# Performance work log

Measured on AMD Instinct MI355X. Metric: run time of the kernel, lower is better.

## Reference

```python
import jax, jax.numpy as jnp
import numpy as np

H = 64
NG = 100000   # gene nodes
ND = 30000    # disease nodes
NE = 1500000  # gda edges (gene -> disease)
NL = 500000   # supervision (label) edges


def setup_inputs() -> dict:
    key = jax.random.key(0)
    ks = jax.random.split(key, 20)
    s = 0.1
    inp = {
        "gene_emb":    jax.random.normal(ks[0], (NG, H), jnp.float32) * s,
        "disease_emb": jax.random.normal(ks[1], (ND, H), jnp.float32) * s,
    }
    wnames = ["w1_gd_l", "w1_gd_r", "w1_dg_l", "w1_dg_r",
              "w2_gd_l", "w2_gd_r", "w2_dg_l", "w2_dg_r"]
    for i, n in enumerate(wnames):
        inp[n] = jax.random.normal(ks[2 + i], (H, H), jnp.float32) * s
    for i, n in enumerate(["b1_gd", "b1_dg", "b2_gd", "b2_dg"]):
        inp[n] = jax.random.normal(ks[10 + i], (H,), jnp.float32) * 0.01
    inp["edge_src"]  = jax.random.randint(ks[14], (NE,), 0, NG)
    inp["edge_dst"]  = jax.random.randint(ks[15], (NE,), 0, ND)
    inp["label_src"] = jax.random.randint(ks[16], (NL,), 0, NG)
    inp["label_dst"] = jax.random.randint(ks[17], (NL,), 0, ND)
    return inp


def _sage(x_src, x_dst, src, dst, n_dst, wl, wr, b):
    # SAGEConv (mean aggr): lin_l(mean_{j in N(i)} x_j) + lin_r(x_i) + b
    msum = jax.ops.segment_sum(x_src[src], dst, num_segments=n_dst)
    cnt = jax.ops.segment_sum(jnp.ones((src.shape[0], 1), x_src.dtype), dst,
                              num_segments=n_dst)
    mean = msum / jnp.maximum(cnt, 1.0)
    return mean @ wl + x_dst @ wr + b


def reference(gene_emb, disease_emb,
              w1_gd_l, w1_gd_r, b1_gd, w1_dg_l, w1_dg_r, b1_dg,
              w2_gd_l, w2_gd_r, b2_gd, w2_dg_l, w2_dg_r, b2_dg,
              edge_src, edge_dst, label_src, label_dst):
    # layer 1 (hetero: gene->disease via gda, disease->gene via rev_gda)
    h_d = jax.nn.relu(_sage(gene_emb, disease_emb, edge_src, edge_dst, ND,
                            w1_gd_l, w1_gd_r, b1_gd))
    h_g = jax.nn.relu(_sage(disease_emb, gene_emb, edge_dst, edge_src, NG,
                            w1_dg_l, w1_dg_r, b1_dg))
    # layer 2 (no activation)
    h_d2 = _sage(h_g, h_d, edge_src, edge_dst, ND, w2_gd_l, w2_gd_r, b2_gd)
    h_g2 = _sage(h_d, h_g, edge_dst, edge_src, NG, w2_dg_l, w2_dg_r, b2_dg)
    # classifier: dot product over label edges
    return jnp.sum(h_g2[label_src] * h_d2[label_dst], axis=-1)
```

## Files before the change

kernel.cpp:

```cpp
#include <hip/hip_runtime.h>
#include <hip/hip_bf16.h>

#define H 64
#define SCAN_CHUNK 512
#define NB1 512

typedef unsigned short u16;
typedef unsigned int u32;
typedef unsigned char u8;
typedef __attribute__((ext_vector_type(8))) __bf16 bf16x8;
typedef __attribute__((ext_vector_type(4))) float f32x4;
typedef __attribute__((ext_vector_type(2))) float f32x2;

__device__ __forceinline__ float bflo(u32 u) {
    return __builtin_bit_cast(float, u << 16);
}
__device__ __forceinline__ float bfhi(u32 u) {
    return __builtin_bit_cast(float, u & 0xffff0000u);
}
__device__ __forceinline__ u16 bf16rne(float f) {
    u32 u = __builtin_bit_cast(u32, f);
    return (u16)((u + 0x7FFFu + ((u >> 16) & 1u)) >> 16);
}
__device__ __forceinline__ u8 fp8enc(float f) {
    return (u8)(__builtin_amdgcn_cvt_pk_fp8_f32(f, 0.0f, 0, false) & 0xFF);
}

__global__ __launch_bounds__(256) void fused_count_convert_kernel(
    const int* __restrict__ es, const int* __restrict__ ed,
    int* __restrict__ histD, int* __restrict__ histG,
    int ne, int shiftD, int shiftG,
    const float* __restrict__ a, u16* __restrict__ oa, u32* __restrict__ oa8,
    long long na4,
    const float* __restrict__ b, u16* __restrict__ ob, u32* __restrict__ ob8,
    long long nb4)
{
    if (blockIdx.x < NB1) {
        __shared__ int lhd[256], lhg[256];
        const int tid = threadIdx.x;
        lhd[tid] = 0; lhg[tid] = 0;
        __syncthreads();
        const int chunk = (ne + NB1 - 1) / NB1;
        const int e0 = blockIdx.x * chunk;
        const int e1 = min(e0 + chunk, ne);
        for (int e = e0 + tid; e < e1; e += 256) {
            atomicAdd(&lhd[ed[e] >> shiftD], 1);
            atomicAdd(&lhg[es[e] >> shiftG], 1);
        }
        __syncthreads();
        histD[tid * NB1 + blockIdx.x] = lhd[tid];
        histG[tid * NB1 + blockIdx.x] = lhg[tid];
        return;
    }
    long long i = (long long)(blockIdx.x - NB1) * 256 + threadIdx.x;
    const float* src; u16* dst; u32* dst8; long long q;
    if (i < na4) { src = a; dst = oa; dst8 = oa8; q = i; }
    else if (i < na4 + nb4) { src = b; dst = ob; dst8 = ob8; q = i - na4; }
    else return;
    float4 v = *(const float4*)&src[q * 4];
    ushort4 o;
    o.x = bf16rne(v.x); o.y = bf16rne(v.y);
    o.z = bf16rne(v.z); o.w = bf16rne(v.w);
    *(ushort4*)&dst[q * 4] = o;
    int r = 0;
    r = __builtin_amdgcn_cvt_pk_fp8_f32(v.x * 16.0f, v.y * 16.0f, r, false);
    r = __builtin_amdgcn_cvt_pk_fp8_f32(v.z * 16.0f, v.w * 16.0f, r, true);
    dst8[q] = (u32)r;
}

__global__ __launch_bounds__(256) void scan_reduce_kernel(
    const int* __restrict__ a1, int n1, const int* __restrict__ a2, int n2,
    int B1, int* __restrict__ partial,
    u32* __restrict__ pad0, u32* __restrict__ pad1,
    u32* __restrict__ pad2, u32* __restrict__ pad3)
{
    if (blockIdx.x == 0) {
        int tz = threadIdx.x;
        if (tz < 16) pad0[tz] = 0;
        else if (tz < 32) pad1[tz - 16] = 0;
        else if (tz < 48) pad2[tz - 32] = 0;
        else if (tz < 64) pad3[tz - 48] = 0;
    }
    const int b = blockIdx.x;
    const int* a; int n, base;
    if (b < B1) { a = a1; n = n1; base = b * SCAN_CHUNK; }
    else        { a = a2; n = n2; base = (b - B1) * SCAN_CHUNK; }
    int t = threadIdx.x;
    int i0 = base + 2 * t, i1 = i0 + 1;
    int v = ((i0 < n) ? a[i0] : 0) + ((i1 < n) ? a[i1] : 0);
    #pragma unroll
    for (int off = 32; off > 0; off >>= 1) v += __shfl_down(v, off, 64);
    __shared__ int ws[4];
    if ((t & 63) == 0) ws[t >> 6] = v;
    __syncthreads();
    if (t == 0) partial[b] = ws[0] + ws[1] + ws[2] + ws[3];
}

__global__ __launch_bounds__(256) void scan_apply_kernel(
    const int* __restrict__ a1, int* __restrict__ out1, int n1,
    const int* __restrict__ a2, int* __restrict__ out2, int n2,
    int B1, int nbtot, const int* __restrict__ partial)
{
    __shared__ int sExcl[1024];
    __shared__ int ws[4];
    const int tid = threadIdx.x;
    const int lane = tid & 63, wid = tid >> 6;

    int j0 = 4 * tid;
    int p0 = (j0 + 0 < nbtot) ? partial[j0 + 0] : 0;
    int p1 = (j0 + 1 < nbtot) ? partial[j0 + 1] : 0;
    int p2 = (j0 + 2 < nbtot) ? partial[j0 + 2] : 0;
    int p3 = (j0 + 3 < nbtot) ? partial[j0 + 3] : 0;
    int psum = p0 + p1 + p2 + p3;
    int P = psum;
    #pragma unroll
    for (int off = 1; off < 64; off <<= 1) {
        int u = __shfl_up(P, off, 64);
        if (lane >= off) P += u;
    }
    if (lane == 63) ws[wid] = P;
    __syncthreads();
    int wbase = 0;
    #pragma unroll
    for (int w = 0; w < 4; ++w) wbase += (w < wid) ? ws[w] : 0;
    int e = wbase + (P - psum);
    sExcl[j0 + 0] = e;
    sExcl[j0 + 1] = e + p0;
    sExcl[j0 + 2] = e + p0 + p1;
    sExcl[j0 + 3] = e + p0 + p1 + p2;
    __syncthreads();

    const int b = blockIdx.x;
    int tot1 = sExcl[B1 - 1] + partial[B1 - 1];
    int myOff = sExcl[b] - ((b >= B1) ? tot1 : 0);
    if (b == 0 && tid == 0) {
        int tot2 = sExcl[nbtot - 1] + partial[nbtot - 1] - tot1;
        out1[n1] = tot1;
        out2[n2] = tot2;
    }
    __syncthreads();

    const int* a; int* out; int n, base;
    if (b < B1) { a = a1; out = out1; n = n1; base = b * SCAN_CHUNK; }
    else        { a = a2; out = out2; n = n2; base = (b - B1) * SCAN_CHUNK; }
    int i0 = base + 2 * tid, i1 = i0 + 1;
    int x0 = (i0 < n) ? a[i0] : 0;
    int x1 = (i1 < n) ? a[i1] : 0;
    int p = x0 + x1;
    int Q = p;
    #pragma unroll
    for (int off = 1; off < 64; off <<= 1) {
        int u = __shfl_up(Q, off, 64);
        if (lane >= off) Q += u;
    }
    if (lane == 63) ws[wid] = Q;
    __syncthreads();
    int waveBase = 0;
    #pragma unroll
    for (int w = 0; w < 4; ++w) waveBase += (w < wid) ? ws[w] : 0;
    int off0 = myOff + waveBase + (Q - p);
    if (i0 < n) out[i0] = off0;
    if (i1 < n) out[i1] = off0 + x0;
}

__global__ __launch_bounds__(256) void part_scatter_kernel(
    const int* __restrict__ es, const int* __restrict__ ed,
    const int* __restrict__ baseD, const int* __restrict__ baseG,
    u32* __restrict__ pairD, u32* __restrict__ pairG,
    int ne, int shiftD, int shiftG)
{
    __shared__ int curD[256], curG[256];
    const int tid = threadIdx.x;
    curD[tid] = baseD[tid * NB1 + blockIdx.x];
    curG[tid] = baseG[tid * NB1 + blockIdx.x];
    __syncthreads();
    const int maskD = (1 << shiftD) - 1;
    const int maskG = (1 << shiftG) - 1;
    const int chunk = (ne + NB1 - 1) / NB1;
    const int e0 = blockIdx.x * chunk;
    const int e1 = min(e0 + chunk, ne);
    for (int e = e0 + tid; e < e1; e += 256) {
        int s = es[e], d = ed[e];
        int pD = atomicAdd(&curD[d >> shiftD], 1);
        pairD[pD] = ((u32)(d & maskD) << 17) | (u32)s;
        int pG = atomicAdd(&curG[s >> shiftG], 1);
        pairG[pG] = ((u32)(s & maskG) << 17) | (u32)d;
    }
}

__global__ __launch_bounds__(256) void csr_build_kernel(
    const u32* __restrict__ pairD, const int* __restrict__ baseD,
    int* __restrict__ rowD, int* __restrict__ idxD, int nd, int shiftD, int nbktD,
    const u32* __restrict__ pairG, const int* __restrict__ baseG,
    int* __restrict__ rowG, int* __restrict__ idxG, int ng, int shiftG, int nbktG)
{
    __shared__ int lcnt[512], lcur[512];
    __shared__ int ws[4];
    const int j = blockIdx.x & 255;
    const int isG = blockIdx.x >> 8;
    const u32* pair; const int* base; int* row; int* idx; int n, shift, nbkt;
    if (isG) { pair = pairG; base = baseG; row = rowG; idx = idxG; n = ng; shift = shiftG; nbkt = nbktG; }
    else     { pair = pairD; base = baseD; row = rowD; idx = idxD; n = nd; shift = shiftD; nbkt = nbktD; }
    if (j >= nbkt) return;

    const int tid = threadIdx.x;
    const int nLo = j << shift;
    const int nHi = min(nLo + (1 << shift), n);
    const int range = nHi - nLo;
    const int segBase = base[j * NB1];
    const int segEnd  = base[(j + 1) * NB1];

    lcnt[tid] = 0; lcnt[tid + 256] = 0;
    __syncthreads();
    for (int t = segBase + tid; t < segEnd; t += 256)
        atomicAdd(&lcnt[pair[t] >> 17], 1);
    __syncthreads();

    int i0 = 2 * tid, i1 = i0 + 1;
    int c0 = (i0 < range) ? lcnt[i0] : 0;
    int c1 = (i1 < range) ? lcnt[i1] : 0;
    int p = c0 + c1;
    int P = p;
    const int lane = tid & 63, wid = tid >> 6;
    #pragma unroll
    for (int off = 1; off < 64; off <<= 1) {
        int u = __shfl_up(P, off, 64);
        if (lane >= off) P += u;
    }
    if (lane == 63) ws[wid] = P;
    __syncthreads();
    int waveBase = 0;
    #pragma unroll
    for (int w = 0; w < 4; ++w) waveBase += (w < wid) ? ws[w] : 0;
    int o0 = segBase + waveBase + (P - p);
    int o1 = o0 + c0;
    if (i0 < range) { row[nLo + i0] = o0; lcur[i0] = o0; }
    if (i1 < range) { row[nLo + i1] = o1; lcur[i1] = o1; }
    if (nHi == n && tid == 0) row[n] = segEnd;
    __syncthreads();

    for (int t = segBase + tid; t < segEnd; t += 256) {
        u32 pr = pair[t];
        int pos = atomicAdd(&lcur[pr >> 17], 1);
        idx[pos] = (int)(pr & 0x1FFFFu);
    }
}

__global__ __launch_bounds__(256) void gather_mean_kernel(
    const u8* __restrict__ srcD, const u8* __restrict__ srcG,
    const int* __restrict__ rowD, const int* __restrict__ idxD,
    const int* __restrict__ rowG, const int* __restrict__ idxG,
    u16* __restrict__ outD, u16* __restrict__ outG, int nd, int ng)
{
    int hw = blockIdx.x * 8 + (threadIdx.x >> 5);
    int l5 = threadIdx.x & 31;
    if (hw >= nd + ng) return;
    const bool isD = hw < nd;
    const int sub = l5 >> 3;
    const int c8 = l5 & 7;
    const u8* src; const int* row; const int* idx; u16* out; int node, npad;
    if (isD) { src = srcD; row = rowD; idx = idxD; out = outD; node = hw;      npad = ng; }
    else     { src = srcG; row = rowG; idx = idxG; out = outG; node = hw - nd; npad = nd; }
    int beg = row[node], end = row[node + 1];
    const u8* srcc = src + c8 * 8;

    f32x2 aA[4], aB[4];
    #pragma unroll
    for (int j = 0; j < 4; ++j) {
        aA[j] = (f32x2){0.f, 0.f}; aB[j] = (f32x2){0.f, 0.f};
    }

    for (int i = beg; i < end; i += 32) {
        int p = i + sub;
        const int* ip = idx + p;
        int t0 = ip[0],  t1 = ip[4],  t2 = ip[8],  t3 = ip[12];
        int t4 = ip[16], t5 = ip[20], t6 = ip[24], t7 = ip[28];
        int s0 = (p      < end) ? t0 : npad;
        int s1 = (p + 4  < end) ? t1 : npad;
        int s2 = (p + 8  < end) ? t2 : npad;
        int s3 = (p + 12 < end) ? t3 : npad;
        int s4 = (p + 16 < end) ? t4 : npad;
        int s5 = (p + 20 < end) ? t5 : npad;
        int s6 = (p + 24 < end) ? t6 : npad;
        int s7 = (p + 28 < end) ? t7 : npad;
        uint2 v0 = *(const uint2*)(srcc + (size_t)s0 * 64);
        uint2 v1 = *(const uint2*)(srcc + (size_t)s1 * 64);
        uint2 v2 = *(const uint2*)(srcc + (size_t)s2 * 64);
        uint2 v3 = *(const uint2*)(srcc + (size_t)s3 * 64);
        uint2 v4 = *(const uint2*)(srcc + (size_t)s4 * 64);
        uint2 v5 = *(const uint2*)(srcc + (size_t)s5 * 64);
        uint2 v6 = *(const uint2*)(srcc + (size_t)s6 * 64);
        uint2 v7 = *(const uint2*)(srcc + (size_t)s7 * 64);
        aA[0] += __builtin_amdgcn_cvt_pk_f32_fp8((int)v0.x, false);
        aA[1] += __builtin_amdgcn_cvt_pk_f32_fp8((int)v0.x, true);
        aA[2] += __builtin_amdgcn_cvt_pk_f32_fp8((int)v0.y, false);
        aA[3] += __builtin_amdgcn_cvt_pk_f32_fp8((int)v0.y, true);
        aA[0] += __builtin_amdgcn_cvt_pk_f32_fp8((int)v1.x, false);
        aA[1] += __builtin_amdgcn_cvt_pk_f32_fp8((int)v1.x, true);
        aA[2] += __builtin_amdgcn_cvt_pk_f32_fp8((int)v1.y, false);
        aA[3] += __builtin_amdgcn_cvt_pk_f32_fp8((int)v1.y, true);
        aA[0] += __builtin_amdgcn_cvt_pk_f32_fp8((int)v2.x, false);
        aA[1] += __builtin_amdgcn_cvt_pk_f32_fp8((int)v2.x, true);
        aA[2] += __builtin_amdgcn_cvt_pk_f32_fp8((int)v2.y, false);
        aA[3] += __builtin_amdgcn_cvt_pk_f32_fp8((int)v2.y, true);
        aA[0] += __builtin_amdgcn_cvt_pk_f32_fp8((int)v3.x, false);
        aA[1] += __builtin_amdgcn_cvt_pk_f32_fp8((int)v3.x, true);
        aA[2] += __builtin_amdgcn_cvt_pk_f32_fp8((int)v3.y, false);
        aA[3] += __builtin_amdgcn_cvt_pk_f32_fp8((int)v3.y, true);
        aB[0] += __builtin_amdgcn_cvt_pk_f32_fp8((int)v4.x, false);
        aB[1] += __builtin_amdgcn_cvt_pk_f32_fp8((int)v4.x, true);
        aB[2] += __builtin_amdgcn_cvt_pk_f32_fp8((int)v4.y, false);
        aB[3] += __builtin_amdgcn_cvt_pk_f32_fp8((int)v4.y, true);
        aB[0] += __builtin_amdgcn_cvt_pk_f32_fp8((int)v5.x, false);
        aB[1] += __builtin_amdgcn_cvt_pk_f32_fp8((int)v5.x, true);
        aB[2] += __builtin_amdgcn_cvt_pk_f32_fp8((int)v5.y, false);
        aB[3] += __builtin_amdgcn_cvt_pk_f32_fp8((int)v5.y, true);
        aB[0] += __builtin_amdgcn_cvt_pk_f32_fp8((int)v6.x, false);
        aB[1] += __builtin_amdgcn_cvt_pk_f32_fp8((int)v6.x, true);
        aB[2] += __builtin_amdgcn_cvt_pk_f32_fp8((int)v6.y, false);
        aB[3] += __builtin_amdgcn_cvt_pk_f32_fp8((int)v6.y, true);
        aB[0] += __builtin_amdgcn_cvt_pk_f32_fp8((int)v7.x, false);
        aB[1] += __builtin_amdgcn_cvt_pk_f32_fp8((int)v7.x, true);
        aB[2] += __builtin_amdgcn_cvt_pk_f32_fp8((int)v7.y, false);
        aB[3] += __builtin_amdgcn_cvt_pk_f32_fp8((int)v7.y, true);
    }

    f32x2 acc[4];
    #pragma unroll
    for (int j = 0; j < 4; ++j) acc[j] = aA[j] + aB[j];
    #pragma unroll
    for (int j = 0; j < 4; ++j) {
        f32x2 t;
        t.x = __shfl_xor(acc[j].x, 8, 64);
        t.y = __shfl_xor(acc[j].y, 8, 64);
        acc[j] += t;
        t.x = __shfl_xor(acc[j].x, 16, 64);
        t.y = __shfl_xor(acc[j].y, 16, 64);
        acc[j] += t;
    }
    if (sub == 0) {
        float inv = 0.0625f / fmaxf((float)(end - beg), 1.0f);
        u32 w0 = (u32)bf16rne(acc[0].x * inv) | ((u32)bf16rne(acc[0].y * inv) << 16);
        u32 w1 = (u32)bf16rne(acc[1].x * inv) | ((u32)bf16rne(acc[1].y * inv) << 16);
        u32 w2 = (u32)bf16rne(acc[2].x * inv) | ((u32)bf16rne(acc[2].y * inv) << 16);
        u32 w3 = (u32)bf16rne(acc[3].x * inv) | ((u32)bf16rne(acc[3].y * inv) << 16);
        uint4 pk = make_uint4(w0, w1, w2, w3);
        *(uint4*)(out + (size_t)node * H + c8 * 8) = pk;
    }
}

template <bool RELU, bool F8OUT>
__global__ __launch_bounds__(256) void sage_mm_mfma_kernel(
    const u16* __restrict__ meanD, const u16* __restrict__ xD, u16* __restrict__ outD,
    u8* __restrict__ outDf8,
    const float* __restrict__ wlD, const float* __restrict__ wrD,
    const float* __restrict__ bD, int nd,
    const u16* __restrict__ meanG, const u16* __restrict__ xG, u16* __restrict__ outG,
    u8* __restrict__ outGf8,
    const float* __restrict__ wlG, const float* __restrict__ wrG,
    const float* __restrict__ bG, int ng, int MBD)
{
    __shared__ u16 sB[16 * 64 * 8];
    int b = blockIdx.x;
    const u16 *mean, *x; u16* out; u8* out8; const float *wl, *wr, *bias; int n;
    if (b < MBD) { mean = meanD; x = xD; out = outD; out8 = outDf8; wl = wlD; wr = wrD; bias = bD; n = nd; }
    else { b -= MBD; mean = meanG; x = xG; out = outG; out8 = outGf8; wl = wlG; wr = wrG; bias = bG; n = ng; }

    const int tid = threadIdx.x;
    for (int i = tid; i < 4096; i += 256) {
        int k = i >> 6, ncol = i & 63;
        int q = (k >> 3) & 3, j = k & 7, t = ncol >> 4, n15 = ncol & 15;
        int lane = q * 16 + n15;
        int c0 = k >> 5;
        sB[(((c0 + 0) * 4 + t) * 64 + lane) * 8 + j] = bf16rne(wl[i]);
        sB[(((c0 + 2) * 4 + t) * 64 + lane) * 8 + j] = bf16rne(wr[i]);
    }
    __syncthreads();

    const int lane = tid & 63;
    const int wave = tid >> 6;
    const int m = lane & 15;
    const int q = lane >> 4;

    bf16x8 Bf[16];
    {
        const uint4* sB4 = (const uint4*)sB;
        #pragma unroll
        for (int f = 0; f < 16; ++f)
            Bf[f] = __builtin_bit_cast(bf16x8, sB4[f * 64 + lane]);
    }
    float bv[4];
    #pragma unroll
    for (int t = 0; t < 4; ++t) bv[t] = bias[t * 16 + m];

    const int row0 = b * 256;
    #pragma unroll
    for (int r = 0; r < 4; ++r) {
        int rbase = row0 + (wave + 4 * r) * 16;
        if (rbase >= n) break;
        int gr = min(rbase + m, n - 1);
        const uint4* mrow = (const uint4*)(mean + (size_t)gr * H);
        const uint4* xrow = (const uint4*)(x + (size_t)gr * H);
        bf16x8 A0 = __builtin_bit_cast(bf16x8, mrow[q]);
        bf16x8 A1 = __builtin_bit_cast(bf16x8, mrow[q + 4]);
        bf16x8 A2 = __builtin_bit_cast(bf16x8, xrow[q]);
        bf16x8 A3 = __builtin_bit_cast(bf16x8, xrow[q + 4]);
        f32x4 acc[4];
        #pragma unroll
        for (int t = 0; t < 4; ++t) acc[t] = (f32x4){bv[t], bv[t], bv[t], bv[t]};
        #pragma unroll
        for (int t = 0; t < 4; ++t) {
            acc[t] = __builtin_amdgcn_mfma_f32_16x16x32_bf16(A0, Bf[0 * 4 + t], acc[t], 0, 0, 0);
            acc[t] = __builtin_amdgcn_mfma_f32_16x16x32_bf16(A1, Bf[1 * 4 + t], acc[t], 0, 0, 0);
            acc[t] = __builtin_amdgcn_mfma_f32_16x16x32_bf16(A2, Bf[2 * 4 + t], acc[t], 0, 0, 0);
            acc[t] = __builtin_amdgcn_mfma_f32_16x16x32_bf16(A3, Bf[3 * 4 + t], acc[t], 0, 0, 0);
        }
        #pragma unroll
        for (int reg = 0; reg < 4; ++reg) {
            int orow = rbase + q * 4 + reg;
            if (orow < n) {
                u16* op = out + (size_t)orow * H;
                u8* op8 = F8OUT ? (out8 + (size_t)orow * H) : nullptr;
                #pragma unroll
                for (int t = 0; t < 4; ++t) {
                    float v = acc[t][reg];
                    if (RELU) v = fmaxf(v, 0.0f);
                    op[t * 16 + m] = bf16rne(v);
                    if (F8OUT) op8[t * 16 + m] = fp8enc(v * 16.0f);
                }
            }
        }
    }
}

__global__ __launch_bounds__(256) void classify_kernel(
    const u16* __restrict__ hg2, const u16* __restrict__ hd2,
    const int* __restrict__ ls, const int* __restrict__ ld,
    float* __restrict__ out, int nl)
{
    long long t = (long long)blockIdx.x * blockDim.x + threadIdx.x;
    int e = (int)(t >> 3);
    int c8 = (int)(t & 7);
    if (e >= nl) return;
    int a = ls[e];
    int b = ld[e];
    uint4 ua = *((const uint4*)(hg2 + (size_t)a * H) + c8);
    uint4 ub = *((const uint4*)(hd2 + (size_t)b * H) + c8);
    float v = bflo(ua.x) * bflo(ub.x) + bfhi(ua.x) * bfhi(ub.x)
            + bflo(ua.y) * bflo(ub.y) + bfhi(ua.y) * bfhi(ub.y)
            + bflo(ua.z) * bflo(ub.z) + bfhi(ua.z) * bfhi(ub.z)
            + bflo(ua.w) * bflo(ub.w) + bfhi(ua.w) * bfhi(ub.w);
    v += __shfl_xor(v, 1, 64);
    v += __shfl_xor(v, 2, 64);
    v += __shfl_xor(v, 4, 64);
    if (c8 == 0) out[e] = v;
}

extern "C" void kernel_launch(void* const* d_in, const int* in_sizes, int n_in,
                              void* d_out, int out_size, void* d_ws, size_t ws_size,
                              hipStream_t stream)
{
    const float* gene  = (const float*)d_in[0];
    const float* dis   = (const float*)d_in[1];
    const float* w1gdl = (const float*)d_in[2];
    const float* w1gdr = (const float*)d_in[3];
    const float* w1dgl = (const float*)d_in[4];
    const float* w1dgr = (const float*)d_in[5];
    const float* w2gdl = (const float*)d_in[6];
    const float* w2gdr = (const float*)d_in[7];
    const float* w2dgl = (const float*)d_in[8];
    const float* w2dgr = (const float*)d_in[9];
    const float* b1gd  = (const float*)d_in[10];
    const float* b1dg  = (const float*)d_in[11];
    const float* b2gd  = (const float*)d_in[12];
    const float* b2dg  = (const float*)d_in[13];
    const int* es = (const int*)d_in[14];
    const int* ed = (const int*)d_in[15];
    const int* ls = (const int*)d_in[16];
    const int* ld = (const int*)d_in[17];

    const int ng = in_sizes[0] / H;
    const int nd = in_sizes[1] / H;
    const int ne = in_sizes[14];
    const int nl = in_sizes[16];

    int shiftD = 0; while (((nd + (1 << shiftD) - 1) >> shiftD) > 256) ++shiftD;
    int shiftG = 0; while (((ng + (1 << shiftG) - 1) >> shiftG) > 256) ++shiftG;
    const int nbktD = (nd + (1 << shiftD) - 1) >> shiftD;
    const int nbktG = (ng + (1 << shiftG) - 1) >> shiftG;
    const int n1 = 256 * NB1;

    int* rowD = (int*)d_ws;
    int* rowG = rowD + nd + 1;
    int* idxD = rowG + ng + 1;
    int* idxG = idxD + ne;
    u16* geneBf = (u16*)(idxG + ne);
    u16* disBf  = geneBf + (size_t)ng * H;
    u16* h1Dbf  = disBf + (size_t)nd * H;
    u16* h1Gbf  = h1Dbf + (size_t)nd * H;
    u16* h2Dbf  = h1Gbf + (size_t)ng * H;
    u16* h2Gbf  = h2Dbf + (size_t)nd * H;
    uintptr_t pf8 = (uintptr_t)(h2Gbf + (size_t)ng * H);
    pf8 = (pf8 + 15) & ~(uintptr_t)15;
    u32* geneF8 = (u32*)pf8;
    u32* disF8  = geneF8 + (size_t)ng * 16 + 16;
    u32* h1DF8  = disF8 + (size_t)nd * 16 + 16;
    u32* h1GF8  = h1DF8 + (size_t)nd * 16 + 16;
    uintptr_t p = (uintptr_t)(h1GF8 + (size_t)ng * 16 + 16);
    p = (p + 15) & ~(uintptr_t)15;
    u16* MD = (u16*)p;
    u16* MG = MD + (size_t)nd * H;
    int* histD = (int*)p;
    int* histG = histD + n1;
    int* baseD = histG + n1;
    int* baseG = baseD + n1 + 1;
    int* partial  = baseG + n1 + 1;
    uintptr_t pp = (uintptr_t)(partial + 1024);
    pp = (pp + 15) & ~(uintptr_t)15;
    u32* pairD = (u32*)pp;
    u32* pairG = pairD + ne;

    const long long na4 = (long long)ng * H / 4;
    const long long nb4 = (long long)nd * H / 4;
    const int convBlocks = (int)((na4 + nb4 + 255) / 256);
    fused_count_convert_kernel<<<NB1 + convBlocks, 256, 0, stream>>>(
        es, ed, histD, histG, ne, shiftD, shiftG,
        gene, geneBf, geneF8, na4, dis, disBf, disF8, nb4);

    const int B1 = n1 / SCAN_CHUNK;
    const int nbtot = 2 * B1;
    scan_reduce_kernel<<<nbtot, 256, 0, stream>>>(histD, n1, histG, n1, B1, partial,
                                                  geneF8 + (size_t)ng * 16,
                                                  disF8 + (size_t)nd * 16,
                                                  h1DF8 + (size_t)nd * 16,
                                                  h1GF8 + (size_t)ng * 16);
    scan_apply_kernel<<<nbtot, 256, 0, stream>>>(histD, baseD, n1,
                                                 histG, baseG, n1, B1, nbtot, partial);

    part_scatter_kernel<<<NB1, 256, 0, stream>>>(es, ed, baseD, baseG,
                                                 pairD, pairG, ne, shiftD, shiftG);
    csr_build_kernel<<<512, 256, 0, stream>>>(
        pairD, baseD, rowD, idxD, nd, shiftD, nbktD,
        pairG, baseG, rowG, idxG, ng, shiftG, nbktG);

    const int gatherBlocks = (nd + ng + 7) / 8;
    const int MBD = (nd + 255) / 256;
    const int MBG = (ng + 255) / 256;

    gather_mean_kernel<<<gatherBlocks, 256, 0, stream>>>(
        (const u8*)geneF8, (const u8*)disF8, rowD, idxD, rowG, idxG, MD, MG, nd, ng);
    sage_mm_mfma_kernel<true, true><<<MBD + MBG, 256, 0, stream>>>(
        MD, disBf, h1Dbf, (u8*)h1DF8, w1gdl, w1gdr, b1gd, nd,
        MG, geneBf, h1Gbf, (u8*)h1GF8, w1dgl, w1dgr, b1dg, ng, MBD);

    gather_mean_kernel<<<gatherBlocks, 256, 0, stream>>>(
        (const u8*)h1GF8, (const u8*)h1DF8, rowD, idxD, rowG, idxG, MD, MG, nd, ng);
    sage_mm_mfma_kernel<false, false><<<MBD + MBG, 256, 0, stream>>>(
        MD, h1Dbf, h2Dbf, nullptr, w2gdl, w2gdr, b2gd, nd,
        MG, h1Gbf, h2Gbf, nullptr, w2dgl, w2dgr, b2dg, ng, MBD);

    {
        long long threads = (long long)nl * 8;
        int blocks = (int)((threads + 255) / 256);
        classify_kernel<<<blocks, 256, 0, stream>>>(h2Gbf, h2Dbf, ls, ld,
                                                    (float*)d_out, nl);
    }
}
```

Baseline: 317.4 us.

## Fuse scan, partition scatter and CSR build into one cooperative kernel

Replaces four separate preprocessing launches (scan reduce, scan apply, partition scatter, CSR build) with a single cooperative kernel of 512 blocks that separates the phases with grid-wide syncs. This removes three kernel launch boundaries and their drain gaps. It relies on nbtot being 512 and on all blocks being co-resident. Grid syncs carry their own cost, and bounds checks on the histogram scan were dropped on the assumption that n1 is a multiple of the chunk size.

```diff
diff --git a/kernel.cpp b/kernel.cpp
--- a/kernel.cpp
+++ b/kernel.cpp
@@ -1,5 +1,8 @@
 #include <hip/hip_runtime.h>
 #include <hip/hip_bf16.h>
+#include <hip/hip_cooperative_groups.h>
+
+namespace cg = cooperative_groups;
 
 #define H 64
 #define SCAN_CHUNK 512
@@ -68,181 +71,176 @@
     dst8[q] = (u32)r;
 }
 
-__global__ __launch_bounds__(256) void scan_reduce_kernel(
-    const int* __restrict__ a1, int n1, const int* __restrict__ a2, int n2,
-    int B1, int* __restrict__ partial,
+__global__ __launch_bounds__(256) void preproc_coop_kernel(
+    int* __restrict__ histD, int* __restrict__ histG, int n1,
+    int* __restrict__ baseD, int* __restrict__ baseG,
+    const int* __restrict__ es, const int* __restrict__ ed,
+    u32* __restrict__ pairD, u32* __restrict__ pairG,
+    int ne, int shiftD, int shiftG,
+    int* __restrict__ rowD, int* __restrict__ idxD, int nd, int nbktD,
+    int* __restrict__ rowG, int* __restrict__ idxG, int ng, int nbktG,
+    int* __restrict__ partial,
     u32* __restrict__ pad0, u32* __restrict__ pad1,
     u32* __restrict__ pad2, u32* __restrict__ pad3)
 {
-    if (blockIdx.x == 0) {
-        int tz = threadIdx.x;
-        if (tz < 16) pad0[tz] = 0;
-        else if (tz < 32) pad1[tz - 16] = 0;
-        else if (tz < 48) pad2[tz - 32] = 0;
-        else if (tz < 64) pad3[tz - 48] = 0;
-    }
+    cg::grid_group grid = cg::this_grid();
+    __shared__ int sh[1028];
+    const int tid = threadIdx.x;
     const int b = blockIdx.x;
-    const int* a; int n, base;
-    if (b < B1) { a = a1; n = n1; base = b * SCAN_CHUNK; }
-    else        { a = a2; n = n2; base = (b - B1) * SCAN_CHUNK; }
-    int t = threadIdx.x;
-    int i0 = base + 2 * t, i1 = i0 + 1;
-    int v = ((i0 < n) ? a[i0] : 0) + ((i1 < n) ? a[i1] : 0);
-    #pragma unroll
-    for (int off = 32; off > 0; off >>= 1) v += __shfl_down(v, off, 64);
-    __shared__ int ws[4];
-    if ((t & 63) == 0) ws[t >> 6] = v;
-    __syncthreads();
-    if (t == 0) partial[b] = ws[0] + ws[1] + ws[2] + ws[3];
-}
-
-__global__ __launch_bounds__(256) void scan_apply_kernel(
-    const int* __restrict__ a1, int* __restrict__ out1, int n1,
-    const int* __restrict__ a2, int* __restrict__ out2, int n2,
-    int B1, int nbtot, const int* __restrict__ partial)
-{
-    __shared__ int sExcl[1024];
-    __shared__ int ws[4];
-    const int tid = threadIdx.x;
     const int lane = tid & 63, wid = tid >> 6;
-
-    int j0 = 4 * tid;
-    int p0 = (j0 + 0 < nbtot) ? partial[j0 + 0] : 0;
-    int p1 = (j0 + 1 < nbtot) ? partial[j0 + 1] : 0;
-    int p2 = (j0 + 2 < nbtot) ? partial[j0 + 2] : 0;
-    int p3 = (j0 + 3 < nbtot) ? partial[j0 + 3] : 0;
-    int psum = p0 + p1 + p2 + p3;
-    int P = psum;
-    #pragma unroll
-    for (int off = 1; off < 64; off <<= 1) {
-        int u = __shfl_up(P, off, 64);
-        if (lane >= off) P += u;
-    }
-    if (lane == 63) ws[wid] = P;
-    __syncthreads();
-    int wbase = 0;
-    #pragma unroll
-    for (int w = 0; w < 4; ++w) wbase += (w < wid) ? ws[w] : 0;
-    int e = wbase + (P - psum);
-    sExcl[j0 + 0] = e;
-    sExcl[j0 + 1] = e + p0;
-    sExcl[j0 + 2] = e + p0 + p1;
-    sExcl[j0 + 3] = e + p0 + p1 + p2;
-    __syncthreads();
-
-    const int b = blockIdx.x;
-    int tot1 = sExcl[B1 - 1] + partial[B1 - 1];
-    int myOff = sExcl[b] - ((b >= B1) ? tot1 : 0);
-    if (b == 0 && tid == 0) {
-        int tot2 = sExcl[nbtot - 1] + partial[nbtot - 1] - tot1;
-        out1[n1] = tot1;
-        out2[n2] = tot2;
-    }
-    __syncthreads();
-
-    const int* a; int* out; int n, base;
-    if (b < B1) { a = a1; out = out1; n = n1; base = b * SCAN_CHUNK; }
-    else        { a = a2; out = out2; n = n2; base = (b - B1) * SCAN_CHUNK; }
-    int i0 = base + 2 * tid, i1 = i0 + 1;
-    int x0 = (i0 < n) ? a[i0] : 0;
-    int x1 = (i1 < n) ? a[i1] : 0;
-    int p = x0 + x1;
-    int Q = p;
-    #pragma unroll
-    for (int off = 1; off < 64; off <<= 1) {
-        int u = __shfl_up(Q, off, 64);
-        if (lane >= off) Q += u;
-    }
-    if (lane == 63) ws[wid] = Q;
-    __syncthreads();
-    int waveBase = 0;
-    #pragma unroll
-    for (int w = 0; w < 4; ++w) waveBase += (w < wid) ? ws[w] : 0;
-    int off0 = myOff + waveBase + (Q - p);
-    if (i0 < n) out[i0] = off0;
-    if (i1 < n) out[i1] = off0 + x0;
-}
-
-__global__ __launch_bounds__(256) void part_scatter_kernel(
-    const int* __restrict__ es, const int* __restrict__ ed,
-    const int* __restrict__ baseD, const int* __restrict__ baseG,
-    u32* __restrict__ pairD, u32* __restrict__ pairG,
-    int ne, int shiftD, int shiftG)
-{
-    __shared__ int curD[256], curG[256];
-    const int tid = threadIdx.x;
-    curD[tid] = baseD[tid * NB1 + blockIdx.x];
-    curG[tid] = baseG[tid * NB1 + blockIdx.x];
-    __syncthreads();
-    const int maskD = (1 << shiftD) - 1;
-    const int maskG = (1 << shiftG) - 1;
-    const int chunk = (ne + NB1 - 1) / NB1;
-    const int e0 = blockIdx.x * chunk;
-    const int e1 = min(e0 + chunk, ne);
-    for (int e = e0 + tid; e < e1; e += 256) {
-        int s = es[e], d = ed[e];
-        int pD = atomicAdd(&curD[d >> shiftD], 1);
-        pairD[pD] = ((u32)(d & maskD) << 17) | (u32)s;
-        int pG = atomicAdd(&curG[s >> shiftG], 1);
-        pairG[pG] = ((u32)(s & maskG) << 17) | (u32)d;
-    }
-}
-
-__global__ __launch_bounds__(256) void csr_build_kernel(
-    const u32* __restrict__ pairD, const int* __restrict__ baseD,
-    int* __restrict__ rowD, int* __restrict__ idxD, int nd, int shiftD, int nbktD,
-    const u32* __restrict__ pairG, const int* __restrict__ baseG,
-    int* __restrict__ rowG, int* __restrict__ idxG, int ng, int shiftG, int nbktG)
-{
-    __shared__ int lcnt[512], lcur[512];
-    __shared__ int ws[4];
-    const int j = blockIdx.x & 255;
-    const int isG = blockIdx.x >> 8;
-    const u32* pair; const int* base; int* row; int* idx; int n, shift, nbkt;
-    if (isG) { pair = pairG; base = baseG; row = rowG; idx = idxG; n = ng; shift = shiftG; nbkt = nbktG; }
-    else     { pair = pairD; base = baseD; row = rowD; idx = idxD; n = nd; shift = shiftD; nbkt = nbktD; }
-    if (j >= nbkt) return;
-
-    const int tid = threadIdx.x;
-    const int nLo = j << shift;
-    const int nHi = min(nLo + (1 << shift), n);
-    const int range = nHi - nLo;
-    const int segBase = base[j * NB1];
-    const int segEnd  = base[(j + 1) * NB1];
-
-    lcnt[tid] = 0; lcnt[tid + 256] = 0;
-    __syncthreads();
-    for (int t = segBase + tid; t < segEnd; t += 256)
-        atomicAdd(&lcnt[pair[t] >> 17], 1);
-    __syncthreads();
-
-    int i0 = 2 * tid, i1 = i0 + 1;
-    int c0 = (i0 < range) ? lcnt[i0] : 0;
-    int c1 = (i1 < range) ? lcnt[i1] : 0;
-    int p = c0 + c1;
-    int P = p;
-    const int lane = tid & 63, wid = tid >> 6;
-    #pragma unroll
-    for (int off = 1; off < 64; off <<= 1) {
-        int u = __shfl_up(P, off, 64);
-        if (lane >= off) P += u;
-    }
-    if (lane == 63) ws[wid] = P;
-    __syncthreads();
-    int waveBase = 0;
-    #pragma unroll
-    for (int w = 0; w < 4; ++w) waveBase += (w < wid) ? ws[w] : 0;
-    int o0 = segBase + waveBase + (P - p);
-    int o1 = o0 + c0;
-    if (i0 < range) { row[nLo + i0] = o0; lcur[i0] = o0; }
-    if (i1 < range) { row[nLo + i1] = o1; lcur[i1] = o1; }
-    if (nHi == n && tid == 0) row[n] = segEnd;
-    __syncthreads();
-
-    for (int t = segBase + tid; t < segEnd; t += 256) {
-        u32 pr = pair[t];
-        int pos = atomicAdd(&lcur[pr >> 17], 1);
-        idx[pos] = (int)(pr & 0x1FFFFu);
+    const int B1 = n1 / SCAN_CHUNK;
+    const int nbtot = 2 * B1;
+
+    {
+        if (b == 0) {
+            if (tid < 16) pad0[tid] = 0;
+            else if (tid < 32) pad1[tid - 16] = 0;
+            else if (tid < 48) pad2[tid - 32] = 0;
+            else if (tid < 64) pad3[tid - 48] = 0;
+        }
+        const int* a = (b < B1) ? histD : histG;
+        int base = ((b < B1) ? b : b - B1) * SCAN_CHUNK;
+        int i0 = base + 2 * tid;
+        int v = a[i0] + a[i0 + 1];
+        #pragma unroll
+        for (int off = 32; off > 0; off >>= 1) v += __shfl_down(v, off, 64);
+        if (lane == 0) sh[1024 + wid] = v;
+        __syncthreads();
+        if (tid == 0) partial[b] = sh[1024] + sh[1025] + sh[1026] + sh[1027];
+    }
+    grid.sync();
+
+    {
+        int* sExcl = sh;
+        int* ws = sh + 1024;
+        int j0 = 4 * tid;
+        int p0 = (j0 + 0 < nbtot) ? partial[j0 + 0] : 0;
+        int p1 = (j0 + 1 < nbtot) ? partial[j0 + 1] : 0;
+        int p2 = (j0 + 2 < nbtot) ? partial[j0 + 2] : 0;
+        int p3 = (j0 + 3 < nbtot) ? partial[j0 + 3] : 0;
+        int psum = p0 + p1 + p2 + p3;
+        int P = psum;
+        #pragma unroll
+        for (int off = 1; off < 64; off <<= 1) {
+            int u = __shfl_up(P, off, 64);
+            if (lane >= off) P += u;
+        }
+        if (lane == 63) ws[wid] = P;
+        __syncthreads();
+        int wbase = 0;
+        #pragma unroll
+        for (int w = 0; w < 4; ++w) wbase += (w < wid) ? ws[w] : 0;
+        int e = wbase + (P - psum);
+        sExcl[j0 + 0] = e;
+        sExcl[j0 + 1] = e + p0;
+        sExcl[j0 + 2] = e + p0 + p1;
+        sExcl[j0 + 3] = e + p0 + p1 + p2;
+        __syncthreads();
+
+        int tot1 = sExcl[B1 - 1] + partial[B1 - 1];
+        int myOff = sExcl[b] - ((b >= B1) ? tot1 : 0);
+        if (b == 0 && tid == 0) {
+            int tot2 = sExcl[nbtot - 1] + partial[nbtot - 1] - tot1;
+            baseD[n1] = tot1;
+            baseG[n1] = tot2;
+        }
+        __syncthreads();
+
+        const int* a; int* out; int base;
+        if (b < B1) { a = histD; out = baseD; base = b * SCAN_CHUNK; }
+        else        { a = histG; out = baseG; base = (b - B1) * SCAN_CHUNK; }
+        int i0 = base + 2 * tid, i1 = i0 + 1;
+        int x0 = a[i0];
+        int x1 = a[i1];
+        int p = x0 + x1;
+        int Q = p;
+        #pragma unroll
+        for (int off = 1; off < 64; off <<= 1) {
+            int u = __shfl_up(Q, off, 64);
+            if (lane >= off) Q += u;
+        }
+        if (lane == 63) ws[wid] = Q;
+        __syncthreads();
+        int waveBase = 0;
+        #pragma unroll
+        for (int w = 0; w < 4; ++w) waveBase += (w < wid) ? ws[w] : 0;
+        int off0 = myOff + waveBase + (Q - p);
+        out[i0] = off0;
+        out[i1] = off0 + x0;
+    }
+    grid.sync();
+
+    {
+        int* curD = sh;
+        int* curG = sh + 256;
+        curD[tid] = baseD[tid * NB1 + b];
+        curG[tid] = baseG[tid * NB1 + b];
+        __syncthreads();
+        const int maskD = (1 << shiftD) - 1;
+        const int maskG = (1 << shiftG) - 1;
+        const int chunk = (ne + NB1 - 1) / NB1;
+        const int e0 = b * chunk;
+        const int e1 = min(e0 + chunk, ne);
+        for (int e = e0 + tid; e < e1; e += 256) {
+            int s = es[e], d = ed[e];
+            int pD = atomicAdd(&curD[d >> shiftD], 1);
+            pairD[pD] = ((u32)(d & maskD) << 17) | (u32)s;
+            int pG = atomicAdd(&curG[s >> shiftG], 1);
+            pairG[pG] = ((u32)(s & maskG) << 17) | (u32)d;
+        }
+    }
+    grid.sync();
+
+    {
+        const int j = b & 255;
+        const int isG = b >> 8;
+        const u32* pair; const int* base; int* row; int* idx; int n, shift, nbkt;
+        if (isG) { pair = pairG; base = baseG; row = rowG; idx = idxG; n = ng; shift = shiftG + 0; nbkt = nbktG; }
+        else     { pair = pairD; base = baseD; row = rowD; idx = idxD; n = nd; shift = shiftD + 0; nbkt = nbktD; }
+        if (j < nbkt) {
+            int* lcnt = sh;
+            int* lcur = sh + 512;
+            int* ws = sh + 1024;
+            const int nLo = j << shift;
+            const int nHi = min(nLo + (1 << shift), n);
+            const int range = nHi - nLo;
+            const int segBase = base[j * NB1];
+            const int segEnd  = base[(j + 1) * NB1];
+
+            lcnt[tid] = 0; lcnt[tid + 256] = 0;
+            __syncthreads();
+            for (int t = segBase + tid; t < segEnd; t += 256)
+                atomicAdd(&lcnt[pair[t] >> 17], 1);
+            __syncthreads();
+
+            int i0 = 2 * tid, i1 = i0 + 1;
+            int c0 = (i0 < range) ? lcnt[i0] : 0;
+            int c1 = (i1 < range) ? lcnt[i1] : 0;
+            int p = c0 + c1;
+            int P = p;
+            #pragma unroll
+            for (int off = 1; off < 64; off <<= 1) {
+                int u = __shfl_up(P, off, 64);
+                if (lane >= off) P += u;
+            }
+            if (lane == 63) ws[wid] = P;
+            __syncthreads();
+            int waveBase = 0;
+            #pragma unroll
+            for (int w = 0; w < 4; ++w) waveBase += (w < wid) ? ws[w] : 0;
+            int o0 = segBase + waveBase + (P - p);
+            int o1 = o0 + c0;
+            if (i0 < range) { row[nLo + i0] = o0; lcur[i0] = o0; }
+            if (i1 < range) { row[nLo + i1] = o1; lcur[i1] = o1; }
+            if (nHi == n && tid == 0) row[n] = segEnd;
+            __syncthreads();
+
+            for (int t = segBase + tid; t < segEnd; t += 256) {
+                u32 pr = pair[t];
+                int pos = atomicAdd(&lcur[pr >> 17], 1);
+                idx[pos] = (int)(pr & 0x1FFFFu);
+            }
+        }
     }
 }
 
@@ -527,21 +525,24 @@
         es, ed, histD, histG, ne, shiftD, shiftG,
         gene, geneBf, geneF8, na4, dis, disBf, disF8, nb4);
 
-    const int B1 = n1 / SCAN_CHUNK;
-    const int nbtot = 2 * B1;
-    scan_reduce_kernel<<<nbtot, 256, 0, stream>>>(histD, n1, histG, n1, B1, partial,
-                                                  geneF8 + (size_t)ng * 16,
-                                                  disF8 + (size_t)nd * 16,
-                                                  h1DF8 + (size_t)nd * 16,
-                                                  h1GF8 + (size_t)ng * 16);
-    scan_apply_kernel<<<nbtot, 256, 0, stream>>>(histD, baseD, n1,
-                                                 histG, baseG, n1, B1, nbtot, partial);
-
-    part_scatter_kernel<<<NB1, 256, 0, stream>>>(es, ed, baseD, baseG,
-                                                 pairD, pairG, ne, shiftD, shiftG);
-    csr_build_kernel<<<512, 256, 0, stream>>>(
-        pairD, baseD, rowD, idxD, nd, shiftD, nbktD,
-        pairG, baseG, rowG, idxG, ng, shiftG, nbktG);
+    {
+        u32* pad0 = geneF8 + (size_t)ng * 16;
+        u32* pad1 = disF8 + (size_t)nd * 16;
+        u32* pad2 = h1DF8 + (size_t)nd * 16;
+        u32* pad3 = h1GF8 + (size_t)ng * 16;
+        int n1v = n1, nev = ne, sDv = shiftD, sGv = shiftG;
+        int ndv = nd, ngv = ng, nbDv = nbktD, nbGv = nbktG;
+        void* args[] = {
+            &histD, &histG, &n1v, &baseD, &baseG,
+            (void*)&es, (void*)&ed, &pairD, &pairG,
+            &nev, &sDv, &sGv,
+            &rowD, &idxD, &ndv, &nbDv,
+            &rowG, &idxG, &ngv, &nbGv,
+            &partial, &pad0, &pad1, &pad2, &pad3
+        };
+        hipLaunchCooperativeKernel((void*)preproc_coop_kernel,
+                                   dim3(512), dim3(256), args, 0, stream);
+    }
 
     const int gatherBlocks = (nd + ng + 7) / 8;
     const int MBD = (nd + 255) / 256;
```

New measurement: 520.8 us. 64.1% more time.

## Replace two-pass bucketed CSR build with direct global-atomic counting sort

Applied to the files above, without the earlier changes.

Swaps the two-level CSR construction (per-block bucket histograms, a partition scatter into pair buffers, then a per-bucket local sort) for a direct scheme. Per-node degrees are counted with global atomics, scanned into row offsets, and edges are scattered straight into idx using global atomic cursors. This removes the intermediate pair buffers and one kernel pass. In exchange it relies on heavy global atomic traffic, and the order of neighbors within each row becomes nondeterministic, which can change float summation order in the gathers.

```diff
diff --git a/kernel.cpp b/kernel.cpp
--- a/kernel.cpp
+++ b/kernel.cpp
@@ -26,33 +26,26 @@
     return (u8)(__builtin_amdgcn_cvt_pk_fp8_f32(f, 0.0f, 0, false) & 0xFF);
 }
 
-__global__ __launch_bounds__(256) void fused_count_convert_kernel(
+__global__ __launch_bounds__(512) void fused_count_convert_kernel(
     const int* __restrict__ es, const int* __restrict__ ed,
-    int* __restrict__ histD, int* __restrict__ histG,
-    int ne, int shiftD, int shiftG,
+    int* __restrict__ cntD, int* __restrict__ cntG,
+    int ne,
     const float* __restrict__ a, u16* __restrict__ oa, u32* __restrict__ oa8,
     long long na4,
     const float* __restrict__ b, u16* __restrict__ ob, u32* __restrict__ ob8,
     long long nb4)
 {
     if (blockIdx.x < NB1) {
-        __shared__ int lhd[256], lhg[256];
-        const int tid = threadIdx.x;
-        lhd[tid] = 0; lhg[tid] = 0;
-        __syncthreads();
         const int chunk = (ne + NB1 - 1) / NB1;
         const int e0 = blockIdx.x * chunk;
         const int e1 = min(e0 + chunk, ne);
-        for (int e = e0 + tid; e < e1; e += 256) {
-            atomicAdd(&lhd[ed[e] >> shiftD], 1);
-            atomicAdd(&lhg[es[e] >> shiftG], 1);
+        for (int e = e0 + (int)threadIdx.x; e < e1; e += 512) {
+            atomicAdd(&cntD[ed[e]], 1);
+            atomicAdd(&cntG[es[e]], 1);
         }
-        __syncthreads();
-        histD[tid * NB1 + blockIdx.x] = lhd[tid];
-        histG[tid * NB1 + blockIdx.x] = lhg[tid];
         return;
     }
-    long long i = (long long)(blockIdx.x - NB1) * 256 + threadIdx.x;
+    long long i = (long long)(blockIdx.x - NB1) * 512 + threadIdx.x;
     const float* src; u16* dst; u32* dst8; long long q;
     if (i < na4) { src = a; dst = oa; dst8 = oa8; q = i; }
     else if (i < na4 + nb4) { src = b; dst = ob; dst8 = ob8; q = i - na4; }
@@ -97,8 +90,8 @@
 }
 
 __global__ __launch_bounds__(256) void scan_apply_kernel(
-    const int* __restrict__ a1, int* __restrict__ out1, int n1,
-    const int* __restrict__ a2, int* __restrict__ out2, int n2,
+    const int* __restrict__ a1, int* __restrict__ out1, int* __restrict__ cur1, int n1,
+    const int* __restrict__ a2, int* __restrict__ out2, int* __restrict__ cur2, int n2,
     int B1, int nbtot, const int* __restrict__ partial)
 {
     __shared__ int sExcl[1024];
@@ -140,9 +133,9 @@
     }
     __syncthreads();
 
-    const int* a; int* out; int n, base;
-    if (b < B1) { a = a1; out = out1; n = n1; base = b * SCAN_CHUNK; }
-    else        { a = a2; out = out2; n = n2; base = (b - B1) * SCAN_CHUNK; }
+    const int* a; int* out; int* cur; int n, base;
+    if (b < B1) { a = a1; out = out1; cur = cur1; n = n1; base = b * SCAN_CHUNK; }
+    else        { a = a2; out = out2; cur = cur2; n = n2; base = (b - B1) * SCAN_CHUNK; }
     int i0 = base + 2 * tid, i1 = i0 + 1;
     int x0 = (i0 < n) ? a[i0] : 0;
     int x1 = (i1 < n) ? a[i1] : 0;
@@ -159,91 +152,22 @@
     #pragma unroll
     for (int w = 0; w < 4; ++w) waveBase += (w < wid) ? ws[w] : 0;
     int off0 = myOff + waveBase + (Q - p);
-    if (i0 < n) out[i0] = off0;
-    if (i1 < n) out[i1] = off0 + x0;
-}
-
-__global__ __launch_bounds__(256) void part_scatter_kernel(
+    if (i0 < n) { out[i0] = off0;      cur[i0] = off0; }
+    if (i1 < n) { out[i1] = off0 + x0; cur[i1] = off0 + x0; }
+}
+
+__global__ __launch_bounds__(512) void scatter_direct_kernel(
     const int* __restrict__ es, const int* __restrict__ ed,
-    const int* __restrict__ baseD, const int* __restrict__ baseG,
-    u32* __restrict__ pairD, u32* __restrict__ pairG,
-    int ne, int shiftD, int shiftG)
-{
-    __shared__ int curD[256], curG[256];
-    const int tid = threadIdx.x;
-    curD[tid] = baseD[tid * NB1 + blockIdx.x];
-    curG[tid] = baseG[tid * NB1 + blockIdx.x];
-    __syncthreads();
-    const int maskD = (1 << shiftD) - 1;
-    const int maskG = (1 << shiftG) - 1;
-    const int chunk = (ne + NB1 - 1) / NB1;
-    const int e0 = blockIdx.x * chunk;
-    const int e1 = min(e0 + chunk, ne);
-    for (int e = e0 + tid; e < e1; e += 256) {
-        int s = es[e], d = ed[e];
-        int pD = atomicAdd(&curD[d >> shiftD], 1);
-        pairD[pD] = ((u32)(d & maskD) << 17) | (u32)s;
-        int pG = atomicAdd(&curG[s >> shiftG], 1);
-        pairG[pG] = ((u32)(s & maskG) << 17) | (u32)d;
-    }
-}
-
-__global__ __launch_bounds__(256) void csr_build_kernel(
-    const u32* __restrict__ pairD, const int* __restrict__ baseD,
-    int* __restrict__ rowD, int* __restrict__ idxD, int nd, int shiftD, int nbktD,
-    const u32* __restrict__ pairG, const int* __restrict__ baseG,
-    int* __restrict__ rowG, int* __restrict__ idxG, int ng, int shiftG, int nbktG)
-{
-    __shared__ int lcnt[512], lcur[512];
-    __shared__ int ws[4];
-    const int j = blockIdx.x & 255;
-    const int isG = blockIdx.x >> 8;
-    const u32* pair; const int* base; int* row; int* idx; int n, shift, nbkt;
-    if (isG) { pair = pairG; base = baseG; row = rowG; idx = idxG; n = ng; shift = shiftG; nbkt = nbktG; }
-    else     { pair = pairD; base = baseD; row = rowD; idx = idxD; n = nd; shift = shiftD; nbkt = nbktD; }
-    if (j >= nbkt) return;
-
-    const int tid = threadIdx.x;
-    const int nLo = j << shift;
-    const int nHi = min(nLo + (1 << shift), n);
-    const int range = nHi - nLo;
-    const int segBase = base[j * NB1];
-    const int segEnd  = base[(j + 1) * NB1];
-
-    lcnt[tid] = 0; lcnt[tid + 256] = 0;
-    __syncthreads();
-    for (int t = segBase + tid; t < segEnd; t += 256)
-        atomicAdd(&lcnt[pair[t] >> 17], 1);
-    __syncthreads();
-
-    int i0 = 2 * tid, i1 = i0 + 1;
-    int c0 = (i0 < range) ? lcnt[i0] : 0;
-    int c1 = (i1 < range) ? lcnt[i1] : 0;
-    int p = c0 + c1;
-    int P = p;
-    const int lane = tid & 63, wid = tid >> 6;
-    #pragma unroll
-    for (int off = 1; off < 64; off <<= 1) {
-        int u = __shfl_up(P, off, 64);
-        if (lane >= off) P += u;
-    }
-    if (lane == 63) ws[wid] = P;
-    __syncthreads();
-    int waveBase = 0;
-    #pragma unroll
-    for (int w = 0; w < 4; ++w) waveBase += (w < wid) ? ws[w] : 0;
-    int o0 = segBase + waveBase + (P - p);
-    int o1 = o0 + c0;
-    if (i0 < range) { row[nLo + i0] = o0; lcur[i0] = o0; }
-    if (i1 < range) { row[nLo + i1] = o1; lcur[i1] = o1; }
-    if (nHi == n && tid == 0) row[n] = segEnd;
-    __syncthreads();
-
-    for (int t = segBase + tid; t < segEnd; t += 256) {
-        u32 pr = pair[t];
-        int pos = atomicAdd(&lcur[pr >> 17], 1);
-        idx[pos] = (int)(pr & 0x1FFFFu);
-    }
+    int* __restrict__ curD, int* __restrict__ curG,
+    int* __restrict__ idxD, int* __restrict__ idxG, int ne)
+{
+    int e = blockIdx.x * 512 + threadIdx.x;
+    if (e >= ne) return;
+    int s = es[e], d = ed[e];
+    int pD = atomicAdd(&curD[d], 1);
+    idxD[pD] = s;
+    int pG = atomicAdd(&curG[s], 1);
+    idxG[pG] = d;
 }
 
 __global__ __launch_bounds__(256) void gather_mean_kernel(
@@ -484,12 +408,6 @@
     const int ne = in_sizes[14];
     const int nl = in_sizes[16];
 
-    int shiftD = 0; while (((nd + (1 << shiftD) - 1) >> shiftD) > 256) ++shiftD;
-    int shiftG = 0; while (((ng + (1 << shiftG) - 1) >> shiftG) > 256) ++shiftG;
-    const int nbktD = (nd + (1 << shiftD) - 1) >> shiftD;
-    const int nbktG = (ng + (1 << shiftG) - 1) >> shiftG;
-    const int n1 = 256 * NB1;
-
     int* rowD = (int*)d_ws;
     int* rowG = rowD + nd + 1;
     int* idxD = rowG + ng + 1;
@@ -510,38 +428,35 @@
     p = (p + 15) & ~(uintptr_t)15;
     u16* MD = (u16*)p;
     u16* MG = MD + (size_t)nd * H;
-    int* histD = (int*)p;
-    int* histG = histD + n1;
-    int* baseD = histG + n1;
-    int* baseG = baseD + n1 + 1;
-    int* partial  = baseG + n1 + 1;
-    uintptr_t pp = (uintptr_t)(partial + 1024);
-    pp = (pp + 15) & ~(uintptr_t)15;
-    u32* pairD = (u32*)pp;
-    u32* pairG = pairD + ne;
+    int* cntD = (int*)p;
+    int* cntG = cntD + nd;
+    int* curD = cntG + ng;
+    int* curG = curD + nd;
+    int* partial = curG + ng;
+
+    hipMemsetAsync(cntD, 0, (size_t)(nd + ng) * sizeof(int), stream);
 
     const long long na4 = (long long)ng * H / 4;
     const long long nb4 = (long long)nd * H / 4;
-    const int convBlocks = (int)((na4 + nb4 + 255) / 256);
-    fused_count_convert_kernel<<<NB1 + convBlocks, 256, 0, stream>>>(
-        es, ed, histD, histG, ne, shiftD, shiftG,
+    const int convBlocks = (int)((na4 + nb4 + 511) / 512);
+    fused_count_convert_kernel<<<NB1 + convBlocks, 512, 0, stream>>>(
+        es, ed, cntD, cntG, ne,
         gene, geneBf, geneF8, na4, dis, disBf, disF8, nb4);
 
-    const int B1 = n1 / SCAN_CHUNK;
-    const int nbtot = 2 * B1;
-    scan_reduce_kernel<<<nbtot, 256, 0, stream>>>(histD, n1, histG, n1, B1, partial,
+    const int B1 = (nd + SCAN_CHUNK - 1) / SCAN_CHUNK;
+    const int B2 = (ng + SCAN_CHUNK - 1) / SCAN_CHUNK;
+    const int nbtot = B1 + B2;
+    scan_reduce_kernel<<<nbtot, 256, 0, stream>>>(cntD, nd, cntG, ng, B1, partial,
                                                   geneF8 + (size_t)ng * 16,
                                                   disF8 + (size_t)nd * 16,
                                                   h1DF8 + (size_t)nd * 16,
                                                   h1GF8 + (size_t)ng * 16);
-    scan_apply_kernel<<<nbtot, 256, 0, stream>>>(histD, baseD, n1,
-                                                 histG, baseG, n1, B1, nbtot, partial);
-
-    part_scatter_kernel<<<NB1, 256, 0, stream>>>(es, ed, baseD, baseG,
-                                                 pairD, pairG, ne, shiftD, shiftG);
-    csr_build_kernel<<<512, 256, 0, stream>>>(
-        pairD, baseD, rowD, idxD, nd, shiftD, nbktD,
-        pairG, baseG, rowG, idxG, ng, shiftG, nbktG);
+    scan_apply_kernel<<<nbtot, 256, 0, stream>>>(cntD, rowD, curD, nd,
+                                                 cntG, rowG, curG, ng,
+                                                 B1, nbtot, partial);
+
+    scatter_direct_kernel<<<(ne + 511) / 512, 512, 0, stream>>>(
+        es, ed, curD, curG, idxD, idxG, ne);
 
     const int gatherBlocks = (nd + ng + 7) / 8;
     const int MBD = (nd + 255) / 256;
```

New measurement: 643.8 us. 2.03x slower.
